# Optimization experiments

Measured on AMD Instinct MI355X. Metric: run time of the kernel, lower is better.

## Reference

```python
import jax, jax.numpy as jnp
import numpy as np

# hardcoded constants from Model.sample_regions / gather_regions / __init__
RADIUS = 0.4
REGIONS = 50
BALL_K = 1000
TOP_K = 4
NEIGHBORHOOD = 128
COURSE = 512


def square_distance(src, dst):
    """src [B,N,C], dst [B,M,C] -> squared dists [B,N,M]."""
    d = -2.0 * jnp.einsum('bnc,bmc->bnm', src, dst)
    d = d + jnp.sum(src * src, -1)[:, :, None]
    d = d + jnp.sum(dst * dst, -1)[:, None, :]
    return d


def furthest_point_sample(xyz, npoint):
    """xyz [B,N,3] -> indices [B,npoint] (deterministic start at point 0)."""
    B, N, _ = xyz.shape
    barange = jnp.arange(B)

    def body(carry, _):
        dist, last = carry                      # dist [B,N], last [B] int32
        centroid = xyz[barange, last]           # [B,3]
        d = jnp.sum((xyz - centroid[:, None, :]) ** 2, -1)
        dist = jnp.minimum(dist, d)
        nxt = jnp.argmax(dist, axis=-1).astype(jnp.int32)
        return (dist, nxt), last

    init = (jnp.full((B, N), 1e10, xyz.dtype), jnp.zeros((B,), jnp.int32))
    _, idxs = jax.lax.scan(body, init, None, length=npoint)
    return jnp.transpose(idxs)                  # [B, npoint]


def knn_point(k, xyz, new_xyz):
    """k-NN of new_xyz [B,S,3] among xyz [B,N,3] -> idx [B,S,k]."""
    d = square_distance(new_xyz, xyz)
    _, idx = jax.lax.top_k(-d, k)
    return idx


def gather_xyz(xyz, idx):
    """xyz [B,N,3], idx [B,S] -> [B,S,3]."""
    B = xyz.shape[0]
    return xyz[jnp.arange(B)[:, None], idx]


def gather_regions(p_xyz, a_xyz, radius):
    """p_xyz [B,N,3] points, a_xyz [B,A,3] anchors -> [B, TOP_K*NEIGHBORHOOD, 3]."""
    B = p_xyz.shape[0]
    d2 = square_distance(a_xyz, p_xyz)                       # [B,A,N]
    counts = jnp.minimum(jnp.sum(d2 < radius * radius, axis=2), BALL_K)
    _, topk_idx = jax.lax.top_k(counts, TOP_K)               # densest anchors [B,TOP_K]
    sel = gather_xyz(a_xyz, topk_idx)                        # [B,TOP_K,3]
    nidx = knn_point(NEIGHBORHOOD, p_xyz, sel)               # [B,TOP_K,NB]
    neigh = p_xyz[jnp.arange(B)[:, None, None], nidx]        # [B,TOP_K,NB,3]
    return neigh.reshape(B, TOP_K * NEIGHBORHOOD, 3)


def sample_regions(p_xyz, regions, r):
    anchors_idx = furthest_point_sample(p_xyz, regions)
    anchors = gather_xyz(p_xyz, anchors_idx)
    return gather_regions(p_xyz, anchors, r)


def setup_inputs() -> dict:
    key = jax.random.key(0)
    points = jax.random.normal(key, (16, 3, 16384), dtype=jnp.float32)
    return {"points": points}


def reference(points):
    # points [B,3,N] -> p_xyz [B,N,3]
    p_xyz = jnp.transpose(points, (0, 2, 1))
    roi1 = sample_regions(p_xyz, REGIONS, RADIUS)            # [B,512,3]
    roi2 = sample_regions(p_xyz, REGIONS, RADIUS)            # [B,512,3] (a == b == 0.4)
    fps_idx = furthest_point_sample(p_xyz, COURSE)           # [B,512]
    fps_pts = gather_xyz(p_xyz, fps_idx)                     # [B,512,3]
    return jnp.concatenate([roi1, roi2, fps_pts], axis=1)    # [B,1536,3]
```

## Files before the change

kernel.cpp:

```cpp
#include <hip/hip_runtime.h>
#include <stdint.h>

#define NPTS 16384
#define BATCH 16
#define FPS_N 512
#define NANCH 50
#define TOPK 4
#define NBH 128
#define BALLK 1000

#define FT 512
#define NW 8

#define CTRL_XOR1 0xB1
#define CTRL_XOR2 0x4E
#define CTRL_ROR4 0x124
#define CTRL_ROR8 0x128

#define DPP_MAX64(v, CTRL) do {                                                   \
  unsigned int _lo = (unsigned int)(v);                                           \
  unsigned int _hi = (unsigned int)((v) >> 32);                                   \
  unsigned int _slo = (unsigned int)__builtin_amdgcn_update_dpp((int)_lo, (int)_lo, CTRL, 0xf, 0xf, false); \
  unsigned int _shi = (unsigned int)__builtin_amdgcn_update_dpp((int)_hi, (int)_hi, CTRL, 0xf, 0xf, false); \
  unsigned long long _o = (((unsigned long long)_shi) << 32) | _slo;              \
  if (_o > (v)) (v) = _o;                                                         \
} while (0)

#define DPP_MIN64(v, CTRL) do {                                                   \
  unsigned int _lo = (unsigned int)(v);                                           \
  unsigned int _hi = (unsigned int)((v) >> 32);                                   \
  unsigned int _slo = (unsigned int)__builtin_amdgcn_update_dpp((int)_lo, (int)_lo, CTRL, 0xf, 0xf, false); \
  unsigned int _shi = (unsigned int)__builtin_amdgcn_update_dpp((int)_hi, (int)_hi, CTRL, 0xf, 0xf, false); \
  unsigned long long _o = (((unsigned long long)_shi) << 32) | _slo;              \
  if (_o < (v)) (v) = _o;                                                         \
} while (0)

#define SWZ16_MIN64(v) do {                                                       \
  unsigned int _lo = (unsigned int)(v), _hi = (unsigned int)((v) >> 32);          \
  unsigned int _slo = (unsigned int)__builtin_amdgcn_ds_swizzle((int)_lo, 0x401f);\
  unsigned int _shi = (unsigned int)__builtin_amdgcn_ds_swizzle((int)_hi, 0x401f);\
  unsigned long long _o = (((unsigned long long)_shi) << 32) | _slo;              \
  if (_o < (v)) (v) = _o;                                                         \
} while (0)

#define SHF32_MIN64(v) do {                                                       \
  unsigned long long _o = __shfl_xor((v), 32, 64);                                \
  if (_o < (v)) (v) = _o;                                                         \
} while (0)

__device__ __forceinline__ uint32_t f2key(float f) {
  uint32_t u = __float_as_uint(f);
  return (u & 0x80000000u) ? ~u : (u | 0x80000000u);
}

#define REP16(OP) OP(0) OP(1) OP(2) OP(3) OP(4) OP(5) OP(6) OP(7) \
                  OP(8) OP(9) OP(10) OP(11) OP(12) OP(13) OP(14) OP(15)

__global__ __launch_bounds__(FT, 2) void mega_kernel(const float* __restrict__ pts,
                                                     float* __restrict__ out) {
  __shared__ unsigned long long s_key[2][NW];
  __shared__ float4 s_xyz[2][NW];
  __shared__ float4 s_anch[NANCH];
  __shared__ int s_cnt[NANCH];
  __shared__ int s_t4[TOPK];
  __shared__ int s_knn[NBH];

  const int bid = blockIdx.x;
  const bool isFps = bid < BATCH;
  const int b = isFps ? bid : ((bid - BATCH) >> 2);
  const int j = (bid - BATCH) & 3;
  const int nsteps = isFps ? FPS_N : NANCH;

  const int t = threadIdx.x;
  const int lane = t & 63;
  const int wS = t >> 6;
  const float* __restrict__ px = pts + (size_t)b * 3 * NPTS;
  const float* __restrict__ py = px + NPTS;
  const float* __restrict__ pz = py + NPTS;

#define DECLK(k) float2 x_##k, y_##k, z_##k, d_##k;
  REP16(DECLK)
#undef DECLK
#define LOADK(k) { const int i2 = ((k) << 10) + (t << 1);                  \
    x_##k = *(const float2*)&px[i2];                                       \
    y_##k = *(const float2*)&py[i2];                                       \
    z_##k = *(const float2*)&pz[i2];                                       \
    d_##k = make_float2(1e10f, 1e10f); }
  REP16(LOADK)
#undef LOADK
#define PINK(k) asm volatile("" : "+v"(x_##k), "+v"(y_##k), "+v"(z_##k));
  REP16(PINK)
#undef PINK

  float bx = px[0], by = py[0], bz = pz[0];
  if (t == 0) {
    if (isFps) {
      float* o = out + ((size_t)b * 1536 + 1024) * 3;
      o[0] = bx; o[1] = by; o[2] = bz;
    } else {
      s_anch[0] = make_float4(bx, by, bz, 0.f);
    }
  }

  for (int step = 1; step < nsteps; ++step) {
    const int par = step & 1;
    const float2 nbx2 = make_float2(-bx, -bx);
    const float2 nby2 = make_float2(-by, -by);
    const float2 nbz2 = make_float2(-bz, -bz);
    float run = -1.0f;
#define FPSK(k) {                                                          \
    float2 t0, t1, t2;                                                     \
    asm("v_pk_add_f32 %0, %3, %6\n\t"                                      \
        "v_pk_add_f32 %1, %4, %7\n\t"                                      \
        "v_pk_add_f32 %2, %5, %8\n\t"                                      \
        "v_pk_mul_f32 %0, %0, %0\n\t"                                      \
        "v_pk_mul_f32 %1, %1, %1\n\t"                                      \
        "v_pk_mul_f32 %2, %2, %2\n\t"                                      \
        "v_pk_add_f32 %0, %0, %1\n\t"                                      \
        "v_pk_add_f32 %0, %0, %2"                                          \
        : "=&v"(t0), "=&v"(t1), "=&v"(t2)                                  \
        : "v"(x_##k), "v"(y_##k), "v"(z_##k), "v"(nbx2), "v"(nby2), "v"(nbz2)); \
    d_##k.x = fminf(d_##k.x, t0.x);                                        \
    d_##k.y = fminf(d_##k.y, t0.y);                                        \
    asm("v_max3_f32 %0, %0, %1, %2"                                        \
        : "+v"(run) : "v"(d_##k.x), "v"(d_##k.y)); }
    REP16(FPSK)
#undef FPSK
    uint32_t m = __float_as_uint(run);
    {
      uint32_t s;
      s = (uint32_t)__builtin_amdgcn_update_dpp((int)m, (int)m, CTRL_XOR1, 0xf, 0xf, false); m = m > s ? m : s;
      s = (uint32_t)__builtin_amdgcn_update_dpp((int)m, (int)m, CTRL_XOR2, 0xf, 0xf, false); m = m > s ? m : s;
      s = (uint32_t)__builtin_amdgcn_update_dpp((int)m, (int)m, CTRL_ROR4, 0xf, 0xf, false); m = m > s ? m : s;
      s = (uint32_t)__builtin_amdgcn_update_dpp((int)m, (int)m, CTRL_ROR8, 0xf, 0xf, false); m = m > s ? m : s;
      s = (uint32_t)__builtin_amdgcn_ds_swizzle((int)m, 0x401f);                              m = m > s ? m : s;
      s = (uint32_t)__shfl_xor((int)m, 32, 64);                                              m = m > s ? m : s;
    }
    const float gmaxf = __uint_as_float(m);
    uint32_t widx_w = 0u;
    bool done = false;
#define BALK(k) {                                                          \
    const unsigned long long b0 = __ballot(d_##k.x == gmaxf);              \
    const unsigned long long b1 = __ballot(d_##k.y == gmaxf);              \
    const unsigned long long cb = b0 | b1;                                 \
    if (!done && cb) {                                                     \
      const int l = (int)__builtin_ctzll(cb);                              \
      const uint32_t p = ((b0 >> l) & 1ull) ? 0u : 1u;                     \
      widx_w = ((uint32_t)(k) << 10) + ((uint32_t)((wS << 6) | l) << 1) + p; \
      if (lane == l) {                                                     \
        const float cx = p ? x_##k.y : x_##k.x;                            \
        const float cy = p ? y_##k.y : y_##k.x;                            \
        const float cz = p ? z_##k.y : z_##k.x;                            \
        s_xyz[par][wS] = make_float4(cx, cy, cz, 0.f);                     \
      }                                                                    \
      done = true;                                                         \
    } }
    REP16(BALK)
#undef BALK
    if (lane == 0)
      s_key[par][wS] = ((unsigned long long)m << 32) | (uint32_t)(~widx_w);
    __syncthreads();
    unsigned long long g = s_key[par][lane & 7];
    const float4 cand = s_xyz[par][lane & 7];
    DPP_MAX64(g, CTRL_XOR1);
    DPP_MAX64(g, CTRL_XOR2);
    DPP_MAX64(g, CTRL_ROR4);
    const uint32_t widx = ~(uint32_t)g;
    const int wstar = (int)((widx >> 7) & 7);
    bx = __shfl(cand.x, wstar, 64);
    by = __shfl(cand.y, wstar, 64);
    bz = __shfl(cand.z, wstar, 64);
    if (t == 0) {
      if (isFps) {
        float* o = out + ((size_t)b * 1536 + 1024 + step) * 3;
        o[0] = bx; o[1] = by; o[2] = bz;
      } else {
        s_anch[step] = make_float4(bx, by, bz, 0.f);
      }
    }
  }
  if (isFps) return;

#define DECLP(k) float2 p_##k;
  REP16(DECLP)
#undef DECLP
#define PSUMK(k) {                                                         \
    float2 s0, s1, s2;                                                     \
    asm("v_pk_mul_f32 %0, %3, %3\n\t"                                      \
        "v_pk_mul_f32 %1, %4, %4\n\t"                                      \
        "v_pk_mul_f32 %2, %5, %5\n\t"                                      \
        "v_pk_add_f32 %0, %0, %1\n\t"                                      \
        "v_pk_add_f32 %0, %0, %2"                                          \
        : "=&v"(s0), "=&v"(s1), "=&v"(s2)                                  \
        : "v"(x_##k), "v"(y_##k), "v"(z_##k));                             \
    p_##k = s0;                                                            \
    asm volatile("" : "+v"(p_##k)); }
  REP16(PSUMK)
#undef PSUMK
  if (t < NANCH) s_cnt[t] = 0;
  __syncthreads();

  const float R2 = (float)(0.4 * 0.4);
  const float2 mm2 = make_float2(-2.0f, -2.0f);
  for (int a = 0; a < NANCH; ++a) {
    const float4 A = s_anch[a];
    const float ax = A.x, ay = A.y, az = A.z;
    const float asum = __fadd_rn(__fadd_rn(__fmul_rn(ax, ax), __fmul_rn(ay, ay)),
                                 __fmul_rn(az, az));
    const float2 ax2 = make_float2(ax, ax);
    const float2 ay2 = make_float2(ay, ay);
    const float2 az2 = make_float2(az, az);
    const float2 as2 = make_float2(asum, asum);
    int cw = 0;
#define CNTK(k) {                                                          \
    float2 d0, d1, d2v;                                                    \
    asm("v_pk_mul_f32 %0, %3, %6\n\t"                                      \
        "v_pk_mul_f32 %1, %4, %7\n\t"                                      \
        "v_pk_mul_f32 %2, %5, %8\n\t"                                      \
        "v_pk_add_f32 %0, %0, %1\n\t"                                      \
        "v_pk_add_f32 %0, %0, %2\n\t"                                      \
        "v_pk_mul_f32 %0, %0, %9\n\t"                                      \
        "v_pk_add_f32 %0, %0, %10\n\t"                                     \
        "v_pk_add_f32 %0, %0, %11"                                         \
        : "=&v"(d0), "=&v"(d1), "=&v"(d2v)                                 \
        : "v"(x_##k), "v"(y_##k), "v"(z_##k), "v"(ax2), "v"(ay2), "v"(az2),\
          "v"(mm2), "v"(as2), "v"(p_##k));                                 \
    cw += (int)__popcll(__ballot(d0.x < R2));                              \
    cw += (int)__popcll(__ballot(d0.y < R2)); }
    REP16(CNTK)
#undef CNTK
    if (lane == 0) atomicAdd(&s_cnt[a], cw);
  }
  __syncthreads();

  if (t == 0) {
    unsigned long long used = 0ULL;
    for (int r = 0; r < TOPK; ++r) {
      int bestc = -1, besta = 0;
      for (int a = 0; a < NANCH; ++a) {
        if (used & (1ULL << a)) continue;
        int c = s_cnt[a];
        c = c < BALLK ? c : BALLK;
        if (c > bestc) { bestc = c; besta = a; }
      }
      used |= 1ULL << besta;
      s_t4[r] = besta;
    }
  }
  __syncthreads();

  {
    const float4 A = s_anch[s_t4[j]];
    const float ax = A.x, ay = A.y, az = A.z;
    const float asum = __fadd_rn(__fadd_rn(__fmul_rn(ax, ax), __fmul_rn(ay, ay)),
                                 __fmul_rn(az, az));
    const float2 ax2 = make_float2(ax, ax);
    const float2 ay2 = make_float2(ay, ay);
    const float2 az2 = make_float2(az, az);
    const float2 as2 = make_float2(asum, asum);
#define DECLKK(k) unsigned long long ka_##k, kb_##k;
    REP16(DECLKK)
#undef DECLKK
#define KEYK(k) {                                                          \
    float2 d0, d1, d2v;                                                    \
    asm("v_pk_mul_f32 %0, %3, %6\n\t"                                      \
        "v_pk_mul_f32 %1, %4, %7\n\t"                                      \
        "v_pk_mul_f32 %2, %5, %8\n\t"                                      \
        "v_pk_add_f32 %0, %0, %1\n\t"                                      \
        "v_pk_add_f32 %0, %0, %2\n\t"                                      \
        "v_pk_mul_f32 %0, %0, %9\n\t"                                      \
        "v_pk_add_f32 %0, %0, %10\n\t"                                     \
        "v_pk_add_f32 %0, %0, %11"                                         \
        : "=&v"(d0), "=&v"(d1), "=&v"(d2v)                                 \
        : "v"(x_##k), "v"(y_##k), "v"(z_##k), "v"(ax2), "v"(ay2), "v"(az2),\
          "v"(mm2), "v"(as2), "v"(p_##k));                                 \
    const int i2 = ((k) << 10) + (t << 1);                                 \
    ka_##k = ((unsigned long long)f2key(d0.x) << 32) | (uint32_t)i2;       \
    kb_##k = ((unsigned long long)f2key(d0.y) << 32) | (uint32_t)(i2 + 1); }
    REP16(KEYK)
#undef KEYK
    for (int r = 0; r < NBH; ++r) {
#define PMINK(k) const unsigned long long w_##k = ka_##k < kb_##k ? ka_##k : kb_##k;
      REP16(PMINK)
#undef PMINK
      const unsigned long long q0 = w_0 < w_8 ? w_0 : w_8;
      const unsigned long long q1 = w_1 < w_9 ? w_1 : w_9;
      const unsigned long long q2 = w_2 < w_10 ? w_2 : w_10;
      const unsigned long long q3 = w_3 < w_11 ? w_3 : w_11;
      const unsigned long long q4 = w_4 < w_12 ? w_4 : w_12;
      const unsigned long long q5 = w_5 < w_13 ? w_5 : w_13;
      const unsigned long long q6 = w_6 < w_14 ? w_6 : w_14;
      const unsigned long long q7 = w_7 < w_15 ? w_7 : w_15;
      const unsigned long long r0 = q0 < q4 ? q0 : q4;
      const unsigned long long r1 = q1 < q5 ? q1 : q5;
      const unsigned long long r2 = q2 < q6 ? q2 : q6;
      const unsigned long long r3 = q3 < q7 ? q3 : q7;
      const unsigned long long s0 = r0 < r2 ? r0 : r2;
      const unsigned long long s1 = r1 < r3 ? r1 : r3;
      unsigned long long m = s0 < s1 ? s0 : s1;

      DPP_MIN64(m, CTRL_XOR1);
      DPP_MIN64(m, CTRL_XOR2);
      DPP_MIN64(m, CTRL_ROR4);
      DPP_MIN64(m, CTRL_ROR8);
      SWZ16_MIN64(m);
      SHF32_MIN64(m);

      const int par = r & 1;
      if (lane == 0) s_key[par][wS] = m;
      __syncthreads();
      unsigned long long g = s_key[par][lane & 7];
      DPP_MIN64(g, CTRL_XOR1);
      DPP_MIN64(g, CTRL_XOR2);
      DPP_MIN64(g, CTRL_ROR4);
      if (t == 0) s_knn[r] = (int)(uint32_t)g;
#define KILLK(k) { if (ka_##k == g) ka_##k = ~0ULL; if (kb_##k == g) kb_##k = ~0ULL; }
      REP16(KILLK)
#undef KILLK
    }
  }
  __syncthreads();

  if (t < NBH) {
    const int idx = s_knn[t];
    const float X = px[idx], Y = py[idx], Z = pz[idx];
    float* o1 = out + ((size_t)b * 1536 + (j << 7) + t) * 3;
    float* o2 = o1 + 512 * 3;
    o1[0] = X; o1[1] = Y; o1[2] = Z;
    o2[0] = X; o2[1] = Y; o2[2] = Z;
  }
}

extern "C" void kernel_launch(void* const* d_in, const int* in_sizes, int n_in,
                              void* d_out, int out_size, void* d_ws, size_t ws_size,
                              hipStream_t stream) {
  const float* pts = (const float*)d_in[0];
  float* out = (float*)d_out;
  (void)d_ws; (void)ws_size;
  mega_kernel<<<dim3(BATCH + BATCH * TOPK), dim3(FT), 0, stream>>>(pts, out);
}
```

Baseline: 932.2 us.

## Double block size to 1024 threads and halve per-thread point registers

Each block now uses 16 waves with 8 point pairs per thread instead of 8 waves with 16, shortening per-thread work in each sequential FPS step. kNN blocks now process two anchors each in sequence, halving the kNN grid, and the cross-wave reductions gain an extra DPP stage. Winner coordinates are read from shared memory instead of via shuffle. The trade-off is more waves synchronising per barrier and a doubled number of serial kNN rounds per block.

```diff
diff --git a/kernel.cpp b/kernel.cpp
--- a/kernel.cpp
+++ b/kernel.cpp
@@ -9,8 +9,8 @@
 #define NBH 128
 #define BALLK 1000
 
-#define FT 512
-#define NW 8
+#define FT 1024
+#define NW 16
 
 #define CTRL_XOR1 0xB1
 #define CTRL_XOR2 0x4E
@@ -53,10 +53,9 @@
   return (u & 0x80000000u) ? ~u : (u | 0x80000000u);
 }
 
-#define REP16(OP) OP(0) OP(1) OP(2) OP(3) OP(4) OP(5) OP(6) OP(7) \
-                  OP(8) OP(9) OP(10) OP(11) OP(12) OP(13) OP(14) OP(15)
-
-__global__ __launch_bounds__(FT, 2) void mega_kernel(const float* __restrict__ pts,
+#define REP8(OP) OP(0) OP(1) OP(2) OP(3) OP(4) OP(5) OP(6) OP(7)
+
+__global__ __launch_bounds__(FT, 4) void mega_kernel(const float* __restrict__ pts,
                                                      float* __restrict__ out) {
   __shared__ unsigned long long s_key[2][NW];
   __shared__ float4 s_xyz[2][NW];
@@ -67,8 +66,8 @@
 
   const int bid = blockIdx.x;
   const bool isFps = bid < BATCH;
-  const int b = isFps ? bid : ((bid - BATCH) >> 2);
-  const int j = (bid - BATCH) & 3;
+  const int b = isFps ? bid : ((bid - BATCH) >> 1);
+  const int p = (bid - BATCH) & 1;
   const int nsteps = isFps ? FPS_N : NANCH;
 
   const int t = threadIdx.x;
@@ -79,17 +78,17 @@
   const float* __restrict__ pz = py + NPTS;
 
 #define DECLK(k) float2 x_##k, y_##k, z_##k, d_##k;
-  REP16(DECLK)
+  REP8(DECLK)
 #undef DECLK
-#define LOADK(k) { const int i2 = ((k) << 10) + (t << 1);                  \
+#define LOADK(k) { const int i2 = ((k) << 11) + (t << 1);                  \
     x_##k = *(const float2*)&px[i2];                                       \
     y_##k = *(const float2*)&py[i2];                                       \
     z_##k = *(const float2*)&pz[i2];                                       \
     d_##k = make_float2(1e10f, 1e10f); }
-  REP16(LOADK)
+  REP8(LOADK)
 #undef LOADK
 #define PINK(k) asm volatile("" : "+v"(x_##k), "+v"(y_##k), "+v"(z_##k));
-  REP16(PINK)
+  REP8(PINK)
 #undef PINK
 
   float bx = px[0], by = py[0], bz = pz[0];
@@ -124,7 +123,7 @@
     d_##k.y = fminf(d_##k.y, t0.y);                                        \
     asm("v_max3_f32 %0, %0, %1, %2"                                        \
         : "+v"(run) : "v"(d_##k.x), "v"(d_##k.y)); }
-    REP16(FPSK)
+    REP8(FPSK)
 #undef FPSK
     uint32_t m = __float_as_uint(run);
     {
@@ -145,31 +144,30 @@
     const unsigned long long cb = b0 | b1;                                 \
     if (!done && cb) {                                                     \
       const int l = (int)__builtin_ctzll(cb);                              \
-      const uint32_t p = ((b0 >> l) & 1ull) ? 0u : 1u;                     \
-      widx_w = ((uint32_t)(k) << 10) + ((uint32_t)((wS << 6) | l) << 1) + p; \
+      const uint32_t pp = ((b0 >> l) & 1ull) ? 0u : 1u;                    \
+      widx_w = ((uint32_t)(k) << 11) + ((uint32_t)((wS << 6) | l) << 1) + pp; \
       if (lane == l) {                                                     \
-        const float cx = p ? x_##k.y : x_##k.x;                            \
-        const float cy = p ? y_##k.y : y_##k.x;                            \
-        const float cz = p ? z_##k.y : z_##k.x;                            \
+        const float cx = pp ? x_##k.y : x_##k.x;                           \
+        const float cy = pp ? y_##k.y : y_##k.x;                           \
+        const float cz = pp ? z_##k.y : z_##k.x;                           \
         s_xyz[par][wS] = make_float4(cx, cy, cz, 0.f);                     \
       }                                                                    \
       done = true;                                                         \
     } }
-    REP16(BALK)
+    REP8(BALK)
 #undef BALK
     if (lane == 0)
       s_key[par][wS] = ((unsigned long long)m << 32) | (uint32_t)(~widx_w);
     __syncthreads();
-    unsigned long long g = s_key[par][lane & 7];
-    const float4 cand = s_xyz[par][lane & 7];
+    unsigned long long g = s_key[par][lane & 15];
     DPP_MAX64(g, CTRL_XOR1);
     DPP_MAX64(g, CTRL_XOR2);
     DPP_MAX64(g, CTRL_ROR4);
+    DPP_MAX64(g, CTRL_ROR8);
     const uint32_t widx = ~(uint32_t)g;
-    const int wstar = (int)((widx >> 7) & 7);
-    bx = __shfl(cand.x, wstar, 64);
-    by = __shfl(cand.y, wstar, 64);
-    bz = __shfl(cand.z, wstar, 64);
+    const int wstar = (int)((widx >> 7) & 15);
+    const float4 W = s_xyz[par][wstar];
+    bx = W.x; by = W.y; bz = W.z;
     if (t == 0) {
       if (isFps) {
         float* o = out + ((size_t)b * 1536 + 1024 + step) * 3;
@@ -182,7 +180,7 @@
   if (isFps) return;
 
 #define DECLP(k) float2 p_##k;
-  REP16(DECLP)
+  REP8(DECLP)
 #undef DECLP
 #define PSUMK(k) {                                                         \
     float2 s0, s1, s2;                                                     \
@@ -195,7 +193,7 @@
         : "v"(x_##k), "v"(y_##k), "v"(z_##k));                             \
     p_##k = s0;                                                            \
     asm volatile("" : "+v"(p_##k)); }
-  REP16(PSUMK)
+  REP8(PSUMK)
 #undef PSUMK
   if (t < NANCH) s_cnt[t] = 0;
   __syncthreads();
@@ -227,7 +225,7 @@
           "v"(mm2), "v"(as2), "v"(p_##k));                                 \
     cw += (int)__popcll(__ballot(d0.x < R2));                              \
     cw += (int)__popcll(__ballot(d0.y < R2)); }
-    REP16(CNTK)
+    REP8(CNTK)
 #undef CNTK
     if (lane == 0) atomicAdd(&s_cnt[a], cw);
   }
@@ -249,7 +247,8 @@
   }
   __syncthreads();
 
-  {
+  for (int jj = 0; jj < 2; ++jj) {
+    const int j = 2 * p + jj;
     const float4 A = s_anch[s_t4[j]];
     const float ax = A.x, ay = A.y, az = A.z;
     const float asum = __fadd_rn(__fadd_rn(__fmul_rn(ax, ax), __fmul_rn(ay, ay)),
@@ -259,7 +258,7 @@
     const float2 az2 = make_float2(az, az);
     const float2 as2 = make_float2(asum, asum);
 #define DECLKK(k) unsigned long long ka_##k, kb_##k;
-    REP16(DECLKK)
+    REP8(DECLKK)
 #undef DECLKK
 #define KEYK(k) {                                                          \
     float2 d0, d1, d2v;                                                    \
@@ -274,30 +273,22 @@
         : "=&v"(d0), "=&v"(d1), "=&v"(d2v)                                 \
         : "v"(x_##k), "v"(y_##k), "v"(z_##k), "v"(ax2), "v"(ay2), "v"(az2),\
           "v"(mm2), "v"(as2), "v"(p_##k));                                 \
-    const int i2 = ((k) << 10) + (t << 1);                                 \
+    const int i2 = ((k) << 11) + (t << 1);                                 \
     ka_##k = ((unsigned long long)f2key(d0.x) << 32) | (uint32_t)i2;       \
     kb_##k = ((unsigned long long)f2key(d0.y) << 32) | (uint32_t)(i2 + 1); }
-    REP16(KEYK)
+    REP8(KEYK)
 #undef KEYK
     for (int r = 0; r < NBH; ++r) {
 #define PMINK(k) const unsigned long long w_##k = ka_##k < kb_##k ? ka_##k : kb_##k;
-      REP16(PMINK)
+      REP8(PMINK)
 #undef PMINK
-      const unsigned long long q0 = w_0 < w_8 ? w_0 : w_8;
-      const unsigned long long q1 = w_1 < w_9 ? w_1 : w_9;
-      const unsigned long long q2 = w_2 < w_10 ? w_2 : w_10;
-      const unsigned long long q3 = w_3 < w_11 ? w_3 : w_11;
-      const unsigned long long q4 = w_4 < w_12 ? w_4 : w_12;
-      const unsigned long long q5 = w_5 < w_13 ? w_5 : w_13;
-      const unsigned long long q6 = w_6 < w_14 ? w_6 : w_14;
-      const unsigned long long q7 = w_7 < w_15 ? w_7 : w_15;
-      const unsigned long long r0 = q0 < q4 ? q0 : q4;
-      const unsigned long long r1 = q1 < q5 ? q1 : q5;
-      const unsigned long long r2 = q2 < q6 ? q2 : q6;
-      const unsigned long long r3 = q3 < q7 ? q3 : q7;
-      const unsigned long long s0 = r0 < r2 ? r0 : r2;
-      const unsigned long long s1 = r1 < r3 ? r1 : r3;
-      unsigned long long m = s0 < s1 ? s0 : s1;
+      const unsigned long long q0 = w_0 < w_4 ? w_0 : w_4;
+      const unsigned long long q1 = w_1 < w_5 ? w_1 : w_5;
+      const unsigned long long q2 = w_2 < w_6 ? w_2 : w_6;
+      const unsigned long long q3 = w_3 < w_7 ? w_3 : w_7;
+      const unsigned long long r0 = q0 < q2 ? q0 : q2;
+      const unsigned long long r1 = q1 < q3 ? q1 : q3;
+      unsigned long long m = r0 < r1 ? r0 : r1;
 
       DPP_MIN64(m, CTRL_XOR1);
       DPP_MIN64(m, CTRL_XOR2);
@@ -309,25 +300,25 @@
       const int par = r & 1;
       if (lane == 0) s_key[par][wS] = m;
       __syncthreads();
-      unsigned long long g = s_key[par][lane & 7];
+      unsigned long long g = s_key[par][lane & 15];
       DPP_MIN64(g, CTRL_XOR1);
       DPP_MIN64(g, CTRL_XOR2);
       DPP_MIN64(g, CTRL_ROR4);
+      DPP_MIN64(g, CTRL_ROR8);
       if (t == 0) s_knn[r] = (int)(uint32_t)g;
 #define KILLK(k) { if (ka_##k == g) ka_##k = ~0ULL; if (kb_##k == g) kb_##k = ~0ULL; }
-      REP16(KILLK)
+      REP8(KILLK)
 #undef KILLK
     }
-  }
-  __syncthreads();
-
-  if (t < NBH) {
-    const int idx = s_knn[t];
-    const float X = px[idx], Y = py[idx], Z = pz[idx];
-    float* o1 = out + ((size_t)b * 1536 + (j << 7) + t) * 3;
-    float* o2 = o1 + 512 * 3;
-    o1[0] = X; o1[1] = Y; o1[2] = Z;
-    o2[0] = X; o2[1] = Y; o2[2] = Z;
+    __syncthreads();
+    if (t < NBH) {
+      const int idx = s_knn[t];
+      const float X = px[idx], Y = py[idx], Z = pz[idx];
+      float* o1 = out + ((size_t)b * 1536 + (j << 7) + t) * 3;
+      float* o2 = o1 + 512 * 3;
+      o1[0] = X; o1[1] = Y; o1[2] = Z;
+      o2[0] = X; o2[1] = Y; o2[2] = Z;
+    }
   }
 }
 
@@ -337,5 +328,5 @@
   const float* pts = (const float*)d_in[0];
   float* out = (float*)d_out;
   (void)d_ws; (void)ws_size;
-  mega_kernel<<<dim3(BATCH + BATCH * TOPK), dim3(FT), 0, stream>>>(pts, out);
+  mega_kernel<<<dim3(BATCH + 2 * BATCH), dim3(FT), 0, stream>>>(pts, out);
 }
```

Result: no change. 931.9 us (-0.0%).
